# Optimization experiments

Hardware: AMD Instinct MI355X
Metric: run time of the kernel (lower is better)

Reference implementation:

```python
import jax, jax.numpy as jnp
import numpy as np

N = 50000   # nodes
E = 800000  # edges (sparse adjacency nnz)
FI = 256    # input feature dim
FO = 64     # output feature dim per head
H = 8       # attention heads


def setup_inputs() -> dict:
    key = jax.random.key(0)
    ks = jax.random.split(key, 6)
    x = jax.random.normal(ks[0], (N, FI), dtype=jnp.float32)
    W = jax.random.normal(ks[1], (H, FI, FO), dtype=jnp.float32) * 0.05
    a = jax.random.normal(ks[2], (H, FO), dtype=jnp.float32) * 0.05
    b = jax.random.normal(ks[3], (H, FO), dtype=jnp.float32) * 0.05
    rows = jax.random.randint(ks[4], (E,), 0, N, dtype=jnp.int32)
    cols = jax.random.randint(ks[5], (E,), 0, N, dtype=jnp.int32)
    return {"x": x, "W": W, "a": a, "b": b, "rows": rows, "cols": cols}


def reference(x, W, a, b, rows, cols):
    # SparseGAT forward: per head linear -> edge scores -> sparse row softmax
    # -> sparse aggregation -> bias; heads averaged then ReLU.
    n = x.shape[0]
    h = W.shape[0]
    NEG_SLOPE = 0.2  # tf.nn.leaky_relu default alpha
    acc = None
    for i in range(h):  # small fixed loop over heads
        t = x @ W[i]                                   # [N, FO]
        aw = t @ a[i]                                  # [N]
        e = jax.nn.leaky_relu(aw[rows] + aw[cols], NEG_SLOPE)   # [E]
        # sparse softmax per row (segment softmax, numerically stable)
        m = jax.ops.segment_max(e, rows, num_segments=n)        # [N]
        ex = jnp.exp(e - m[rows])                                # [E]
        den = jax.ops.segment_sum(ex, rows, num_segments=n)      # [N]
        coef = ex / den[rows]                                    # [E]
        # sparse matmul: sum_j coef_ij * t_j
        agg = jax.ops.segment_sum(coef[:, None] * t[cols], rows, num_segments=n)
        agg = agg + b[i]
        acc = agg if acc is None else acc + agg
    return jax.nn.relu(acc / h)
```

## Files before the change

### kernel.cpp

```cpp
#include <hip/hip_runtime.h>
#include <hip/hip_bf16.h>
#include <hip/hip_fp16.h>


#define FI 256
#define FO 64
#define NH 8
#define FC 512
#define BM 128
#define NBIN 64

typedef _Float16 f16x8 __attribute__((ext_vector_type(8)));
typedef float f32x16 __attribute__((ext_vector_type(16)));
typedef float f32x8 __attribute__((ext_vector_type(8)));

__global__ __launch_bounds__(256)
void p1_wconv(const float* __restrict__ W, _Float16* __restrict__ Wth) {
  int idx = blockIdx.x * 256 + threadIdx.x;
  if (idx >= NH * FO * FI) return;
  int k = idx & (FI - 1);
  int f = (idx >> 8) & (FO - 1);
  int h = idx >> 14;
  Wth[idx] = (_Float16)W[((size_t)h * FI + k) * FO + f];
}

__global__ __launch_bounds__(512)
void k1_v2(const float* __restrict__ x, const _Float16* __restrict__ Wth,
           const float* __restrict__ a, _Float16* __restrict__ Th2,
           float* __restrict__ aw, int N) {
  __shared__ _Float16 smem[BM * 136];
  auto Xs = reinterpret_cast<_Float16(*)[136]>(smem);
  auto Tt = reinterpret_cast<_Float16(*)[512]>(smem);
  const int bm = blockIdx.x * BM;
  const int t = threadIdx.x;
  const int w = t >> 6;
  const int lane = t & 63;
  const int l31 = lane & 31;
  const int kh = (lane >> 5) * 8;
  const _Float16* Wh = Wth + (size_t)w * (FO * FI);

  f32x16 acc[4][2];
  #pragma unroll
  for (int mr = 0; mr < 4; ++mr)
    #pragma unroll
    for (int wc = 0; wc < 2; ++wc) acc[mr][wc] = (f32x16)0.0f;

  #pragma unroll
  for (int k0 = 0; k0 < 2; ++k0) {
    if (k0) __syncthreads();
    #pragma unroll
    for (int r = 0; r < 8; ++r) {
      int i = t + r * 512;
      int row = i >> 5;
      int q = i & 31;
      float4 v = make_float4(0.f, 0.f, 0.f, 0.f);
      if (bm + row < N)
        v = reinterpret_cast<const float4*>(&x[(size_t)(bm + row) * FI + k0 * 128])[q];
      _Float16 o[4] = {(_Float16)v.x, (_Float16)v.y, (_Float16)v.z, (_Float16)v.w};
      *reinterpret_cast<uint2*>(&Xs[row][q * 4]) = *reinterpret_cast<uint2*>(o);
    }
    __syncthreads();
    #pragma unroll
    for (int kk = 0; kk < 8; ++kk) {
      f16x8 af[4], bf[2];
      #pragma unroll
      for (int mr = 0; mr < 4; ++mr)
        af[mr] = *reinterpret_cast<const f16x8*>(&Xs[mr * 32 + l31][kk * 16 + kh]);
      #pragma unroll
      for (int wc = 0; wc < 2; ++wc)
        bf[wc] = *reinterpret_cast<const f16x8*>(
            &Wh[(size_t)(wc * 32 + l31) * FI + k0 * 128 + kk * 16 + kh]);
      #pragma unroll
      for (int mr = 0; mr < 4; ++mr)
        #pragma unroll
        for (int wc = 0; wc < 2; ++wc)
          acc[mr][wc] =
              __builtin_amdgcn_mfma_f32_32x32x16_f16(af[mr], bf[wc], acc[mr][wc], 0, 0, 0);
    }
  }

  const float av0 = a[w * FO + l31], av1 = a[w * FO + 32 + l31];
  #pragma unroll
  for (int mr = 0; mr < 4; ++mr)
    #pragma unroll
    for (int reg = 0; reg < 16; ++reg) {
      float s = acc[mr][0][reg] * av0 + acc[mr][1][reg] * av1;
      #pragma unroll
      for (int off = 1; off < 32; off <<= 1) s += __shfl_xor(s, off);
      if (l31 == 0) {
        int rl = mr * 32 + (reg & 3) + 8 * (reg >> 2) + 4 * (lane >> 5);
        if (bm + rl < N) aw[(size_t)(bm + rl) * NH + w] = s;
      }
    }

  #pragma unroll
  for (int ch = 0; ch < 4; ++ch) {
    __syncthreads();
    #pragma unroll
    for (int wc = 0; wc < 2; ++wc) {
      const int f = wc * 32 + l31;
      #pragma unroll
      for (int reg = 0; reg < 16; ++reg) {
        int rl = (reg & 3) + 8 * (reg >> 2) + 4 * (lane >> 5);
        Tt[rl][f * NH + w] = (_Float16)acc[ch][wc][reg];
      }
    }
    __syncthreads();
    #pragma unroll
    for (int r = 0; r < 4; ++r) {
      int i = t + r * 512;
      int row = i >> 6, q = i & 63;
      int grow = bm + ch * 32 + row;
      if (grow < N)
        *reinterpret_cast<uint4*>(&Th2[(size_t)grow * FC + q * 8]) =
            *reinterpret_cast<const uint4*>(&Tt[row][q * 8]);
    }
  }
}

__global__ __launch_bounds__(256)
void b1_hist(const int* __restrict__ rows, int* __restrict__ deg, int E) {
  int e = blockIdx.x * 256 + threadIdx.x;
  if (e < E) atomicAdd(&deg[rows[e]], 1);
}

__global__ __launch_bounds__(256)
void b2a_blocksum(const int* __restrict__ deg, int* __restrict__ blocksums, int N) {
  __shared__ int red[256];
  const int t = threadIdx.x;
  const int base = blockIdx.x * 1024 + t * 4;
  int s = 0;
  #pragma unroll
  for (int j = 0; j < 4; ++j) { int i = base + j; if (i < N) s += deg[i]; }
  red[t] = s;
  __syncthreads();
  for (int off = 128; off; off >>= 1) {
    if (t < off) red[t] += red[t + off];
    __syncthreads();
  }
  if (t == 0) blocksums[blockIdx.x] = red[0];
}

__global__ __launch_bounds__(64)
void b2b_scanblocks(int* __restrict__ blocksums, int nb,
                    int* __restrict__ row_start, int N, int E) {
  const int lane = threadIdx.x;
  int carry = 0;
  for (int base = 0; base < nb; base += 64) {
    int i = base + lane;
    int v = (i < nb) ? blocksums[i] : 0;
    int inc = v;
    #pragma unroll
    for (int off = 1; off < 64; off <<= 1) {
      int t = __shfl_up(inc, off);
      if (lane >= off) inc += t;
    }
    if (i < nb) blocksums[i] = inc - v + carry;
    carry += __shfl(inc, 63);
  }
  if (lane == 0) row_start[N] = E;
}

__global__ __launch_bounds__(256)
void b2c_rescan(const int* __restrict__ deg, const int* __restrict__ blocksums,
                int* __restrict__ row_start, int* __restrict__ cursor, int N) {
  __shared__ int ts[256];
  const int t = threadIdx.x;
  const int base = blockIdx.x * 1024 + t * 4;
  int v[4]; int s = 0;
  #pragma unroll
  for (int j = 0; j < 4; ++j) { int i = base + j; v[j] = (i < N) ? deg[i] : 0; s += v[j]; }
  ts[t] = s;
  __syncthreads();
  for (int off = 1; off < 256; off <<= 1) {
    int add = (t >= off) ? ts[t - off] : 0;
    __syncthreads();
    ts[t] += add;
    __syncthreads();
  }
  int run = blocksums[blockIdx.x] + ts[t] - s;
  #pragma unroll
  for (int j = 0; j < 4; ++j) {
    int i = base + j;
    if (i < N) { row_start[i] = run; cursor[i] = run; run += v[j]; }
  }
}

__global__ __launch_bounds__(256)
void b3_scatter(const int* __restrict__ rows, const int* __restrict__ cols,
                int* __restrict__ cursor, int* __restrict__ colperm, int E) {
  int e = blockIdx.x * 256 + threadIdx.x;
  if (e >= E) return;
  int pos = atomicAdd(&cursor[rows[e]], 1);
  colperm[pos] = cols[e];
}

__global__ __launch_bounds__(256)
void b5a_hist(const int* __restrict__ deg, int* __restrict__ blockhist,
              int N, int nbp) {
  __shared__ int hist[NBIN];
  const int t = threadIdx.x;
  if (t < NBIN) hist[t] = 0;
  __syncthreads();
  const int base = blockIdx.x * 1024 + t * 4;
  #pragma unroll
  for (int j = 0; j < 4; ++j) {
    int i = base + j;
    if (i < N) atomicAdd(&hist[min(deg[i], NBIN - 1)], 1);
  }
  __syncthreads();
  if (t < NBIN) blockhist[t * nbp + blockIdx.x] = hist[t];
}

__global__ __launch_bounds__(64)
void b5b_scan(int* __restrict__ blockhist, int nbp) {
  const int lane = threadIdx.x;
  int* rowp = blockhist + lane * nbp;
  int tot = 0;
  for (int c = 0; c < nbp / 4; ++c) {
    int4 v = reinterpret_cast<const int4*>(rowp)[c];
    tot += v.x + v.y + v.z + v.w;
  }
  int inc = tot;
  #pragma unroll
  for (int off = 1; off < 64; off <<= 1) {
    int t = __shfl_up(inc, off);
    if (lane >= off) inc += t;
  }
  int run = inc - tot;
  for (int c = 0; c < nbp / 4; ++c) {
    int4 v = reinterpret_cast<const int4*>(rowp)[c];
    int4 o;
    o.x = run; run += v.x;
    o.y = run; run += v.y;
    o.z = run; run += v.z;
    o.w = run; run += v.w;
    reinterpret_cast<int4*>(rowp)[c] = o;
  }
}

__global__ __launch_bounds__(256)
void b5c_scatter(const int* __restrict__ deg, const int* __restrict__ blockhist,
                 int* __restrict__ row_order, int N, int nbp) {
  __shared__ int cur[NBIN];
  const int t = threadIdx.x;
  if (t < NBIN) cur[t] = blockhist[t * nbp + blockIdx.x];
  __syncthreads();
  const int base = blockIdx.x * 1024 + t * 4;
  #pragma unroll
  for (int j = 0; j < 4; ++j) {
    int i = base + j;
    if (i < N) {
      int pos = atomicAdd(&cur[min(deg[i], NBIN - 1)], 1);
      row_order[pos] = i;
    }
  }
}

__global__ __launch_bounds__(256)
void k4_fused(const int* __restrict__ row_start, const int* __restrict__ colperm,
              const int* __restrict__ row_order,
              const float* __restrict__ aw, const _Float16* __restrict__ Th2,
              const float* __restrict__ b, float* __restrict__ out, int N) {
  const int lane16 = threadIdx.x & 15;
  const int gbase  = threadIdx.x & 48;
  const int ri = blockIdx.x * 16 + (threadIdx.x >> 4);
  if (ri >= N) return;
  const int r = row_order[ri];

  const int s0 = row_start[r], s1 = row_start[r + 1];
  f32x8 awr = *reinterpret_cast<const f32x8*>(&aw[(size_t)r * NH]);

  float facc[4][NH] = {};
  float dacc[NH] = {};

  for (int base = s0; base < s1; base += 16) {
    const int mm = min(16, s1 - base);
    const bool valid = lane16 < mm;
    int c_l = valid ? colperm[base + lane16] : 0;

    f32x8 awc = *reinterpret_cast<const f32x8*>(&aw[(size_t)c_l * NH]);
    float ex[NH];
    #pragma unroll
    for (int h = 0; h < NH; ++h) {
      float s = awr[h] + awc[h];
      float lr = s > 0.f ? s : 0.2f * s;
      ex[h] = valid ? __expf(lr) : 0.f;
      dacc[h] += ex[h];
    }

    for (int j = 0; j < mm; ++j) {
      int cj = __shfl(c_l, gbase + j);
      const _Float16* tp = Th2 + (size_t)cj * FC + lane16 * NH;
      f16x8 tv0 = *reinterpret_cast<const f16x8*>(tp);
      f16x8 tv1 = *reinterpret_cast<const f16x8*>(tp + 128);
      f16x8 tv2 = *reinterpret_cast<const f16x8*>(tp + 256);
      f16x8 tv3 = *reinterpret_cast<const f16x8*>(tp + 384);
      #pragma unroll
      for (int h = 0; h < NH; ++h) {
        float e = __shfl(ex[h], gbase + j);
        facc[0][h] = fmaf(e, (float)tv0[h], facc[0][h]);
        facc[1][h] = fmaf(e, (float)tv1[h], facc[1][h]);
        facc[2][h] = fmaf(e, (float)tv2[h], facc[2][h]);
        facc[3][h] = fmaf(e, (float)tv3[h], facc[3][h]);
      }
    }
  }

  #pragma unroll
  for (int h = 0; h < NH; ++h) {
    #pragma unroll
    for (int off = 1; off < 16; off <<= 1)
      dacc[h] += __shfl_xor(dacc[h], off);
  }

  float rden[NH];
  #pragma unroll
  for (int h = 0; h < NH; ++h) rden[h] = dacc[h] > 0.f ? 1.0f / dacc[h] : 0.f;

  #pragma unroll
  for (int q = 0; q < 4; ++q) {
    const int f = q * 16 + lane16;
    float sb = 0.f;
    #pragma unroll
    for (int h = 0; h < NH; ++h) sb += b[h * FO + f];
    float v = 0.f;
    #pragma unroll
    for (int h = 0; h < NH; ++h) v += facc[q][h] * rden[h];
    v = (v + sb) * 0.125f;
    out[(size_t)r * FO + f] = v > 0.f ? v : 0.f;
  }
}

extern "C" void kernel_launch(void* const* d_in, const int* in_sizes, int n_in,
                              void* d_out, int out_size, void* d_ws, size_t ws_size,
                              hipStream_t stream) {
  const float* x    = (const float*)d_in[0];
  const float* W    = (const float*)d_in[1];
  const float* a    = (const float*)d_in[2];
  const float* b    = (const float*)d_in[3];
  const int*   rows = (const int*)d_in[4];
  const int*   cols = (const int*)d_in[5];
  const int N = in_sizes[0] / FI;
  const int E = in_sizes[4];

  const int nb  = (N + 1023) / 1024;
  const int nbp = ((nb + 3) / 4) * 4;

  char* p = (char*)d_ws;
  _Float16* Th2      = (_Float16*)p;  p += (size_t)N * FC * sizeof(_Float16);
  _Float16* Wth      = (_Float16*)p;  p += (size_t)NH * FO * FI * sizeof(_Float16);
  float*    aw       = (float*)p;     p += (size_t)N * NH * sizeof(float);
  int*      deg      = (int*)p;       p += (size_t)N * sizeof(int);
  int*      row_start= (int*)p;       p += (size_t)(N + 4) * sizeof(int);
  int*      cursor   = (int*)p;       p += (size_t)N * sizeof(int);
  int*      colperm  = (int*)p;       p += (size_t)E * sizeof(int);
  int*      blocksums= (int*)p;       p += 64 * sizeof(int);
  int*      row_order= (int*)p;       p += (size_t)N * sizeof(int);
  int*      blockhist= (int*)p;       p += (size_t)NBIN * nbp * sizeof(int);
  float*    out = (float*)d_out;

  hipMemsetAsync(deg, 0, (size_t)N * sizeof(int), stream);
  hipMemsetAsync(blockhist, 0, (size_t)NBIN * nbp * sizeof(int), stream);
  b1_hist<<<(E + 255) / 256, 256, 0, stream>>>(rows, deg, E);
  b2a_blocksum<<<nb, 256, 0, stream>>>(deg, blocksums, N);
  b2b_scanblocks<<<1, 64, 0, stream>>>(blocksums, nb, row_start, N, E);
  b2c_rescan<<<nb, 256, 0, stream>>>(deg, blocksums, row_start, cursor, N);
  b3_scatter<<<(E + 255) / 256, 256, 0, stream>>>(rows, cols, cursor, colperm, E);

  b5a_hist<<<nb, 256, 0, stream>>>(deg, blockhist, N, nbp);
  b5b_scan<<<1, 64, 0, stream>>>(blockhist, nbp);
  b5c_scatter<<<nb, 256, 0, stream>>>(deg, blockhist, row_order, N, nbp);

  p1_wconv<<<(NH * FO * FI + 255) / 256, 256, 0, stream>>>(W, Wth);
  k1_v2<<<(N + BM - 1) / BM, 512, 0, stream>>>(x, Wth, a, Th2, aw, N);

  k4_fused<<<(N + 15) / 16, 256, 0, stream>>>(row_start, colperm, row_order,
                                              aw, Th2, b, out, N);
}
```

Baseline: 303.2 us.

## Store T head-major from MFMA registers, pack edge weights as half2, fuse degree histogram

The projection kernel swaps the MFMA operands so that each lane holds a contiguous run of features for one node. It then writes T directly to global memory in head-major layout, dropping the LDS transpose and its barriers, and computes aw with a single cross-half shuffle instead of a 5-step reduction. The aggregation kernel now reads head-contiguous T. It packs the per-edge softmax weights as half2, cutting shuffles per neighbour from 8 to 4, and adds one cross-lane reduction at the end. The degree histogram is folded into the rescan kernel, removing one launch. The costs are fp16 rounding of the attention weights and uint2 stores from lanes that may coalesce less well.

```diff
diff --git a/kernel.cpp b/kernel.cpp
--- a/kernel.cpp
+++ b/kernel.cpp
@@ -25,18 +25,17 @@
 }
 
 __global__ __launch_bounds__(512)
-void k1_v2(const float* __restrict__ x, const _Float16* __restrict__ Wth,
-           const float* __restrict__ a, _Float16* __restrict__ Th2,
+void k1_v3(const float* __restrict__ x, const _Float16* __restrict__ Wth,
+           const float* __restrict__ a, _Float16* __restrict__ Th,
            float* __restrict__ aw, int N) {
-  __shared__ _Float16 smem[BM * 136];
-  auto Xs = reinterpret_cast<_Float16(*)[136]>(smem);
-  auto Tt = reinterpret_cast<_Float16(*)[512]>(smem);
+  __shared__ _Float16 Xs[BM][136];
   const int bm = blockIdx.x * BM;
   const int t = threadIdx.x;
   const int w = t >> 6;
   const int lane = t & 63;
   const int l31 = lane & 31;
-  const int kh = (lane >> 5) * 8;
+  const int hi = lane >> 5;
+  const int kh = hi * 8;
   const _Float16* Wh = Wth + (size_t)w * (FO * FI);
 
   f32x16 acc[4][2];
@@ -62,59 +61,57 @@
     __syncthreads();
     #pragma unroll
     for (int kk = 0; kk < 8; ++kk) {
-      f16x8 af[4], bf[2];
+      f16x8 xf[4], wf[2];
       #pragma unroll
       for (int mr = 0; mr < 4; ++mr)
-        af[mr] = *reinterpret_cast<const f16x8*>(&Xs[mr * 32 + l31][kk * 16 + kh]);
+        xf[mr] = *reinterpret_cast<const f16x8*>(&Xs[mr * 32 + l31][kk * 16 + kh]);
       #pragma unroll
       for (int wc = 0; wc < 2; ++wc)
-        bf[wc] = *reinterpret_cast<const f16x8*>(
+        wf[wc] = *reinterpret_cast<const f16x8*>(
             &Wh[(size_t)(wc * 32 + l31) * FI + k0 * 128 + kk * 16 + kh]);
       #pragma unroll
       for (int mr = 0; mr < 4; ++mr)
         #pragma unroll
         for (int wc = 0; wc < 2; ++wc)
           acc[mr][wc] =
-              __builtin_amdgcn_mfma_f32_32x32x16_f16(af[mr], bf[wc], acc[mr][wc], 0, 0, 0);
-    }
-  }
-
-  const float av0 = a[w * FO + l31], av1 = a[w * FO + 32 + l31];
-  #pragma unroll
-  for (int mr = 0; mr < 4; ++mr)
+              __builtin_amdgcn_mfma_f32_32x32x16_f16(wf[wc], xf[mr], acc[mr][wc], 0, 0, 0);
+    }
+  }
+
+
+  float s4[4] = {0.f, 0.f, 0.f, 0.f};
+  #pragma unroll
+  for (int wc = 0; wc < 2; ++wc)
     #pragma unroll
     for (int reg = 0; reg < 16; ++reg) {
-      float s = acc[mr][0][reg] * av0 + acc[mr][1][reg] * av1;
-      #pragma unroll
-      for (int off = 1; off < 32; off <<= 1) s += __shfl_xor(s, off);
-      if (l31 == 0) {
-        int rl = mr * 32 + (reg & 3) + 8 * (reg >> 2) + 4 * (lane >> 5);
-        if (bm + rl < N) aw[(size_t)(bm + rl) * NH + w] = s;
+      float av = a[w * FO + wc * 32 + (reg & 3) + 8 * (reg >> 2) + 4 * hi];
+      #pragma unroll
+      for (int mr = 0; mr < 4; ++mr)
+        s4[mr] = fmaf(acc[mr][wc][reg], av, s4[mr]);
+    }
+  #pragma unroll
+  for (int mr = 0; mr < 4; ++mr) {
+    float s = s4[mr] + __shfl_xor(s4[mr], 32);
+    int n = bm + mr * 32 + l31;
+    if (hi == 0 && n < N) aw[(size_t)n * NH + w] = s;
+  }
+
+  #pragma unroll
+  for (int mr = 0; mr < 4; ++mr) {
+    int n = bm + mr * 32 + l31;
+    if (n >= N) continue;
+    _Float16* rowp = Th + (size_t)n * FC + w * FO;
+    #pragma unroll
+    for (int wc = 0; wc < 2; ++wc)
+      #pragma unroll
+      for (int g = 0; g < 4; ++g) {
+        _Float16 o[4] = {(_Float16)acc[mr][wc][4 * g + 0],
+                         (_Float16)acc[mr][wc][4 * g + 1],
+                         (_Float16)acc[mr][wc][4 * g + 2],
+                         (_Float16)acc[mr][wc][4 * g + 3]};
+        *reinterpret_cast<uint2*>(&rowp[wc * 32 + 8 * g + 4 * hi]) =
+            *reinterpret_cast<uint2*>(o);
       }
-    }
-
-  #pragma unroll
-  for (int ch = 0; ch < 4; ++ch) {
-    __syncthreads();
-    #pragma unroll
-    for (int wc = 0; wc < 2; ++wc) {
-      const int f = wc * 32 + l31;
-      #pragma unroll
-      for (int reg = 0; reg < 16; ++reg) {
-        int rl = (reg & 3) + 8 * (reg >> 2) + 4 * (lane >> 5);
-        Tt[rl][f * NH + w] = (_Float16)acc[ch][wc][reg];
-      }
-    }
-    __syncthreads();
-    #pragma unroll
-    for (int r = 0; r < 4; ++r) {
-      int i = t + r * 512;
-      int row = i >> 6, q = i & 63;
-      int grow = bm + ch * 32 + row;
-      if (grow < N)
-        *reinterpret_cast<uint4*>(&Th2[(size_t)grow * FC + q * 8]) =
-            *reinterpret_cast<const uint4*>(&Tt[row][q * 8]);
-    }
   }
 }
 
@@ -163,10 +160,13 @@
 
 __global__ __launch_bounds__(256)
 void b2c_rescan(const int* __restrict__ deg, const int* __restrict__ blocksums,
-                int* __restrict__ row_start, int* __restrict__ cursor, int N) {
+                int* __restrict__ row_start, int* __restrict__ cursor,
+                int* __restrict__ blockhist, int N, int nbp) {
   __shared__ int ts[256];
+  __shared__ int hist[NBIN];
   const int t = threadIdx.x;
   const int base = blockIdx.x * 1024 + t * 4;
+  if (t < NBIN) hist[t] = 0;
   int v[4]; int s = 0;
   #pragma unroll
   for (int j = 0; j < 4; ++j) { int i = base + j; v[j] = (i < N) ? deg[i] : 0; s += v[j]; }
@@ -182,8 +182,13 @@
   #pragma unroll
   for (int j = 0; j < 4; ++j) {
     int i = base + j;
-    if (i < N) { row_start[i] = run; cursor[i] = run; run += v[j]; }
-  }
+    if (i < N) {
+      row_start[i] = run; cursor[i] = run; run += v[j];
+      atomicAdd(&hist[min(v[j], NBIN - 1)], 1);
+    }
+  }
+  __syncthreads();
+  if (t < NBIN) blockhist[t * nbp + blockIdx.x] = hist[t];
 }
 
 __global__ __launch_bounds__(256)
@@ -193,23 +198,6 @@
   if (e >= E) return;
   int pos = atomicAdd(&cursor[rows[e]], 1);
   colperm[pos] = cols[e];
-}
-
-__global__ __launch_bounds__(256)
-void b5a_hist(const int* __restrict__ deg, int* __restrict__ blockhist,
-              int N, int nbp) {
-  __shared__ int hist[NBIN];
-  const int t = threadIdx.x;
-  if (t < NBIN) hist[t] = 0;
-  __syncthreads();
-  const int base = blockIdx.x * 1024 + t * 4;
-  #pragma unroll
-  for (int j = 0; j < 4; ++j) {
-    int i = base + j;
-    if (i < N) atomicAdd(&hist[min(deg[i], NBIN - 1)], 1);
-  }
-  __syncthreads();
-  if (t < NBIN) blockhist[t * nbp + blockIdx.x] = hist[t];
 }
 
 __global__ __launch_bounds__(64)
@@ -260,10 +248,11 @@
 __global__ __launch_bounds__(256)
 void k4_fused(const int* __restrict__ row_start, const int* __restrict__ colperm,
               const int* __restrict__ row_order,
-              const float* __restrict__ aw, const _Float16* __restrict__ Th2,
+              const float* __restrict__ aw, const _Float16* __restrict__ Th,
               const float* __restrict__ b, float* __restrict__ out, int N) {
   const int lane16 = threadIdx.x & 15;
   const int gbase  = threadIdx.x & 48;
+  const int hi8    = lane16 >> 3;
   const int ri = blockIdx.x * 16 + (threadIdx.x >> 4);
   if (ri >= N) return;
   const int r = row_order[ri];
@@ -271,7 +260,7 @@
   const int s0 = row_start[r], s1 = row_start[r + 1];
   f32x8 awr = *reinterpret_cast<const f32x8*>(&aw[(size_t)r * NH]);
 
-  float facc[4][NH] = {};
+  float facc[4][8] = {};
   float dacc[NH] = {};
 
   for (int base = s0; base < s1; base += 16) {
@@ -281,6 +270,7 @@
 
     f32x8 awc = *reinterpret_cast<const f32x8*>(&aw[(size_t)c_l * NH]);
     float ex[NH];
+    int pkv[4];
     #pragma unroll
     for (int h = 0; h < NH; ++h) {
       float s = awr[h] + awc[h];
@@ -288,21 +278,32 @@
       ex[h] = valid ? __expf(lr) : 0.f;
       dacc[h] += ex[h];
     }
+    #pragma unroll
+    for (int q = 0; q < 4; ++q) {
+      __half2 h2 = __floats2half2_rn(ex[2 * q], ex[2 * q + 1]);
+      pkv[q] = *reinterpret_cast<int*>(&h2);
+    }
 
     for (int j = 0; j < mm; ++j) {
       int cj = __shfl(c_l, gbase + j);
-      const _Float16* tp = Th2 + (size_t)cj * FC + lane16 * NH;
+      const _Float16* tp = Th + (size_t)cj * FC + lane16 * 8;
       f16x8 tv0 = *reinterpret_cast<const f16x8*>(tp);
       f16x8 tv1 = *reinterpret_cast<const f16x8*>(tp + 128);
       f16x8 tv2 = *reinterpret_cast<const f16x8*>(tp + 256);
       f16x8 tv3 = *reinterpret_cast<const f16x8*>(tp + 384);
-      #pragma unroll
-      for (int h = 0; h < NH; ++h) {
-        float e = __shfl(ex[h], gbase + j);
-        facc[0][h] = fmaf(e, (float)tv0[h], facc[0][h]);
-        facc[1][h] = fmaf(e, (float)tv1[h], facc[1][h]);
-        facc[2][h] = fmaf(e, (float)tv2[h], facc[2][h]);
-        facc[3][h] = fmaf(e, (float)tv3[h], facc[3][h]);
+      float eq[4];
+      #pragma unroll
+      for (int q = 0; q < 4; ++q) {
+        int p = __shfl(pkv[q], gbase + j);
+        float2 f2 = __half22float2(*reinterpret_cast<__half2*>(&p));
+        eq[q] = hi8 ? f2.y : f2.x;
+      }
+      #pragma unroll
+      for (int e = 0; e < 8; ++e) {
+        facc[0][e] = fmaf(eq[0], (float)tv0[e], facc[0][e]);
+        facc[1][e] = fmaf(eq[1], (float)tv1[e], facc[1][e]);
+        facc[2][e] = fmaf(eq[2], (float)tv2[e], facc[2][e]);
+        facc[3][e] = fmaf(eq[3], (float)tv3[e], facc[3][e]);
       }
     }
   }
@@ -313,22 +314,30 @@
     for (int off = 1; off < 16; off <<= 1)
       dacc[h] += __shfl_xor(dacc[h], off);
   }
-
   float rden[NH];
   #pragma unroll
   for (int h = 0; h < NH; ++h) rden[h] = dacc[h] > 0.f ? 1.0f / dacc[h] : 0.f;
 
+  float s[8] = {};
   #pragma unroll
   for (int q = 0; q < 4; ++q) {
-    const int f = q * 16 + lane16;
-    float sb = 0.f;
-    #pragma unroll
-    for (int h = 0; h < NH; ++h) sb += b[h * FO + f];
-    float v = 0.f;
-    #pragma unroll
-    for (int h = 0; h < NH; ++h) v += facc[q][h] * rden[h];
-    v = (v + sb) * 0.125f;
-    out[(size_t)r * FO + f] = v > 0.f ? v : 0.f;
+    float rd = hi8 ? rden[2 * q + 1] : rden[2 * q];
+    #pragma unroll
+    for (int e = 0; e < 8; ++e) s[e] = fmaf(facc[q][e], rd, s[e]);
+  }
+  #pragma unroll
+  for (int e = 0; e < 8; ++e) s[e] += __shfl_xor(s[e], 8);
+
+  if (lane16 < 8) {
+    #pragma unroll
+    for (int e = 0; e < 8; ++e) {
+      const int f = lane16 * 8 + e;
+      float sb = 0.f;
+      #pragma unroll
+      for (int h = 0; h < NH; ++h) sb += b[h * FO + f];
+      float v = (s[e] + sb) * 0.125f;
+      out[(size_t)r * FO + f] = v > 0.f ? v : 0.f;
+    }
   }
 }
 
@@ -348,7 +357,7 @@
   const int nbp = ((nb + 3) / 4) * 4;
 
   char* p = (char*)d_ws;
-  _Float16* Th2      = (_Float16*)p;  p += (size_t)N * FC * sizeof(_Float16);
+  _Float16* Th       = (_Float16*)p;  p += (size_t)N * FC * sizeof(_Float16);
   _Float16* Wth      = (_Float16*)p;  p += (size_t)NH * FO * FI * sizeof(_Float16);
   float*    aw       = (float*)p;     p += (size_t)N * NH * sizeof(float);
   int*      deg      = (int*)p;       p += (size_t)N * sizeof(int);
@@ -365,16 +374,15 @@
   b1_hist<<<(E + 255) / 256, 256, 0, stream>>>(rows, deg, E);
   b2a_blocksum<<<nb, 256, 0, stream>>>(deg, blocksums, N);
   b2b_scanblocks<<<1, 64, 0, stream>>>(blocksums, nb, row_start, N, E);
-  b2c_rescan<<<nb, 256, 0, stream>>>(deg, blocksums, row_start, cursor, N);
+  b2c_rescan<<<nb, 256, 0, stream>>>(deg, blocksums, row_start, cursor,
+                                     blockhist, N, nbp);
   b3_scatter<<<(E + 255) / 256, 256, 0, stream>>>(rows, cols, cursor, colperm, E);
-
-  b5a_hist<<<nb, 256, 0, stream>>>(deg, blockhist, N, nbp);
   b5b_scan<<<1, 64, 0, stream>>>(blockhist, nbp);
   b5c_scatter<<<nb, 256, 0, stream>>>(deg, blockhist, row_order, N, nbp);
 
   p1_wconv<<<(NH * FO * FI + 255) / 256, 256, 0, stream>>>(W, Wth);
-  k1_v2<<<(N + BM - 1) / BM, 512, 0, stream>>>(x, Wth, a, Th2, aw, N);
+  k1_v3<<<(N + BM - 1) / BM, 512, 0, stream>>>(x, Wth, a, Th, aw, N);
 
   k4_fused<<<(N + 15) / 16, 256, 0, stream>>>(row_start, colperm, row_order,
-                                              aw, Th2, b, out, N);
-}
+                                              aw, Th, b, out, N);
+}
```

Result: faster. 285.2 us (-5.9%).
